# Kernel tuning notes

Hardware: AMD Instinct MI355X
Metric: run time of the kernel (lower is better)

## Reference

```python
import jax, jax.numpy as jnp
import numpy as np

NEG_INF = -1e30  # stand-in for float('-inf') masked_fill (safe for softmax)


def setup_inputs() -> dict:
    key = jax.random.key(0)
    ks = jax.random.split(key, 7)
    B, T, C, H, D = 4, 2048, 64, 6, 64
    s = 1.0 / np.sqrt(C)
    return {
        "x": jax.random.normal(ks[0], (B, T, C), dtype=jnp.float32),
        "y": jax.random.normal(ks[1], (B, T, C), dtype=jnp.float32),
        "Wq": jax.random.normal(ks[2], (H, C, D), dtype=jnp.float32) * s,
        "Wk": jax.random.normal(ks[3], (H, C, D), dtype=jnp.float32) * s,
        "Wv": jax.random.normal(ks[4], (H, C, D), dtype=jnp.float32) * s,
        "W_proj": jax.random.normal(ks[5], (H * D, C), dtype=jnp.float32) * (1.0 / np.sqrt(H * D)),
        "b_proj": jnp.zeros((C,), dtype=jnp.float32),
    }


def reference(x, y, Wq, Wk, Wv, W_proj, b_proj):
    # x, y: [B, T, C]; per-head projections stacked over H (heads vectorized).
    B, T, C = x.shape
    H, _, D = Wq.shape
    q = jnp.einsum("btc,hcd->bhtd", x, Wq)   # query from decoder input x
    k = jnp.einsum("btc,hcd->bhtd", y, Wk)   # key from encoder output y
    v = jnp.einsum("btc,hcd->bhtd", y, Wv)
    scale = D ** (-0.5)
    wei = jnp.einsum("bhtd,bhsd->bhts", q, k) * scale  # [B,H,T,T]
    # triu(ones(T,T), diagonal=1) future mask (causal)
    future = jnp.triu(jnp.ones((T, T), dtype=bool), k=1)
    wei = jnp.where(future, NEG_INF, wei)
    wei = jax.nn.softmax(wei, axis=-1)  # dropout = identity in eval
    out = jnp.einsum("bhts,bhsd->bhtd", wei, v)          # [B,H,T,D]
    out = out.transpose(0, 2, 1, 3).reshape(B, T, H * D)  # concat heads
    return out @ W_proj + b_proj                          # [B,T,C]
```

## Files before the change

### kernel.cpp

```cpp
#include <hip/hip_runtime.h>


typedef unsigned short u16t;
typedef __attribute__((ext_vector_type(8))) short short8;
typedef __attribute__((ext_vector_type(4))) float float4v;

#define MFMA16(a, b, c) __builtin_amdgcn_mfma_f32_16x16x32_bf16((a), (b), (c), 0, 0, 0)

union U8 { short8 s; unsigned u[4]; };

__device__ __forceinline__ float fexp2(float x) {
  return __builtin_amdgcn_exp2f(x);
}
__device__ __forceinline__ float bf2f(u16t u) {
  return __uint_as_float(((unsigned)u) << 16);
}
__device__ __forceinline__ u16t f2bf(float f) {
  unsigned u = __float_as_uint(f);
  u += 0x7fffu + ((u >> 16) & 1u);
  return (u16t)(u >> 16);
}
__device__ __forceinline__ unsigned bftr(float f) {
  return __float_as_uint(f) >> 16;
}
__device__ __forceinline__ short8 load8_f32_bf16(const float* p) {
  float4 f0 = *(const float4*)p;
  float4 f1 = *(const float4*)(p + 4);
  short8 r;
  r[0] = (short)f2bf(f0.x); r[1] = (short)f2bf(f0.y);
  r[2] = (short)f2bf(f0.z); r[3] = (short)f2bf(f0.w);
  r[4] = (short)f2bf(f1.x); r[5] = (short)f2bf(f1.y);
  r[6] = (short)f2bf(f1.z); r[7] = (short)f2bf(f1.w);
  return r;
}

constexpr int Bb = 4, Tt = 2048, Cc = 64, Hh = 6, Dd = 64;
constexpr int BH = Bb * Hh;
constexpr int NQT = Tt / 64;
constexpr int LDT = 72;
constexpr int LDV = 136;
constexpr int OST = 68;
#define QSCALE (0.125f * 1.44269504088896f)

__global__ __launch_bounds__(256) void qkv_kernel(
    const float* __restrict__ x, const float* __restrict__ y,
    const float* __restrict__ Wq, const float* __restrict__ Wk,
    const float* __restrict__ Wv,
    u16t* __restrict__ Q, u16t* __restrict__ K, u16t* __restrict__ Vt) {
  __shared__ __align__(16) u16t wtq[64 * LDT];
  __shared__ __align__(16) u16t wtk[64 * LDT];
  __shared__ __align__(16) u16t wtv[64 * LDT];

  int bid = blockIdx.x;
  int bh = bid >> 5, tt = bid & 31;
  int b = bh / Hh, h = bh - b * Hh;
  int tid = threadIdx.x;
  int w = tid >> 6, lane = tid & 63;
  int l15 = lane & 15, q4 = lane >> 4;

  {
    const float4* wq4 = (const float4*)(Wq + h * 4096);
    const float4* wk4 = (const float4*)(Wk + h * 4096);
    const float4* wv4 = (const float4*)(Wv + h * 4096);
#pragma unroll
    for (int i = 0; i < 4; ++i) {
      int fidx = tid + i * 256;
      float4 qv = wq4[fidx], kv = wk4[fidx], vv = wv4[fidx];
      int base = fidx * 4;
      int c = base >> 6, d0 = base & 63;
      wtq[(d0 + 0) * LDT + c] = f2bf(qv.x);
      wtq[(d0 + 1) * LDT + c] = f2bf(qv.y);
      wtq[(d0 + 2) * LDT + c] = f2bf(qv.z);
      wtq[(d0 + 3) * LDT + c] = f2bf(qv.w);
      wtk[(d0 + 0) * LDT + c] = f2bf(kv.x);
      wtk[(d0 + 1) * LDT + c] = f2bf(kv.y);
      wtk[(d0 + 2) * LDT + c] = f2bf(kv.z);
      wtk[(d0 + 3) * LDT + c] = f2bf(kv.w);
      wtv[(d0 + 0) * LDT + c] = f2bf(vv.x);
      wtv[(d0 + 1) * LDT + c] = f2bf(vv.y);
      wtv[(d0 + 2) * LDT + c] = f2bf(vv.z);
      wtv[(d0 + 3) * LDT + c] = f2bf(vv.w);
    }
  }

  int trow = tt * 64 + w * 16 + l15;
  const float* xrow = x + ((size_t)b * Tt + trow) * Cc;
  const float* yrow = y + ((size_t)b * Tt + trow) * Cc;
  short8 xa[2], ya[2];
#pragma unroll
  for (int kc = 0; kc < 2; ++kc) {
    xa[kc] = load8_f32_bf16(xrow + kc * 32 + q4 * 8);
    ya[kc] = load8_f32_bf16(yrow + kc * 32 + q4 * 8);
  }
  __syncthreads();

  float4v qa4[4], ka4[4], va4[4];
#pragma unroll
  for (int nc = 0; nc < 4; ++nc) {
    qa4[nc] = (float4v){0.f, 0.f, 0.f, 0.f};
    ka4[nc] = (float4v){0.f, 0.f, 0.f, 0.f};
    va4[nc] = (float4v){0.f, 0.f, 0.f, 0.f};
  }
#pragma unroll
  for (int nc = 0; nc < 4; ++nc) {
#pragma unroll
    for (int kc = 0; kc < 2; ++kc) {
      int off = (nc * 16 + l15) * LDT + kc * 32 + q4 * 8;
      short8 bq = *(const short8*)&wtq[off];
      short8 bk = *(const short8*)&wtk[off];
      short8 bv = *(const short8*)&wtv[off];
      qa4[nc] = MFMA16(xa[kc], bq, qa4[nc]);
      ka4[nc] = MFMA16(ya[kc], bk, ka4[nc]);
      va4[nc] = MFMA16(ya[kc], bv, va4[nc]);
    }
  }
  __syncthreads();

#pragma unroll
  for (int reg = 0; reg < 4; ++reg) {
    int rloc = w * 16 + q4 * 4 + reg;
#pragma unroll
    for (int nc = 0; nc < 4; ++nc) {
      wtq[rloc * LDT + nc * 16 + l15] = f2bf(qa4[nc][reg] * QSCALE);
      wtk[rloc * LDT + nc * 16 + l15] = f2bf(ka4[nc][reg]);
      wtv[(nc * 16 + l15) * LDT + rloc] = f2bf(va4[nc][reg]);
    }
  }
  __syncthreads();

  size_t tilebase = ((size_t)bh * Tt + tt * 64) * Dd;
#pragma unroll
  for (int i = 0; i < 2; ++i) {
    int id = tid * 2 + i;
    int row = id >> 3, c8 = id & 7;
    *(uint4*)&Q[tilebase + row * 64 + c8 * 8] = *(const uint4*)&wtq[row * LDT + c8 * 8];
    *(uint4*)&K[tilebase + row * 64 + c8 * 8] = *(const uint4*)&wtk[row * LDT + c8 * 8];
    *(uint4*)&Vt[((size_t)bh * 64 + row) * Tt + tt * 64 + c8 * 8] =
        *(const uint4*)&wtv[row * LDT + c8 * 8];
  }
}

__global__ __launch_bounds__(256) void attn_kernel(
    const u16t* __restrict__ Q, const u16t* __restrict__ K,
    const u16t* __restrict__ Vt, u16t* __restrict__ att) {
  __shared__ __align__(16) unsigned char smem[128 * LDT * 2 + 64 * LDV * 2];
  u16t* Kl = (u16t*)smem;
  u16t* Vl = (u16t*)(smem + 128 * LDT * 2);
  float* Ol = (float*)smem;
  float* Ll = (float*)(smem + 64 * OST * 4);

  int bid = blockIdx.x;
  int bh = bid % BH;
  int qt = (NQT - 1) - bid / BH;
  int b = bh / Hh, h = bh - (bh / Hh) * Hh;
  int tid = threadIdx.x;
  int w = tid >> 6;
  int lane = tid & 63;
  int l15 = lane & 15, q4 = lane >> 4;

  short8 qf[4][2];
#pragma unroll
  for (int it = 0; it < 4; ++it) {
    const u16t* qb = Q + ((size_t)bh * Tt + qt * 64 + it * 16 + l15) * Dd;
    qf[it][0] = *(const short8*)(qb + q4 * 8);
    qf[it][1] = *(const short8*)(qb + 32 + q4 * 8);
  }

  float4v O[4][4];
#pragma unroll
  for (int it = 0; it < 4; ++it)
#pragma unroll
    for (int nc = 0; nc < 4; ++nc) O[it][nc] = (float4v){0.f, 0.f, 0.f, 0.f};
  float l_[4] = {0.f, 0.f, 0.f, 0.f};

  const u16t* Kbh = K + (size_t)bh * Tt * Dd;
  const u16t* Vbh = Vt + (size_t)bh * Dd * Tt;
  const int bsmax = qt >> 1;

  for (int bs = 0; bs <= bsmax; ++bs) {
    __syncthreads();
    {
      const u16t* ks = Kbh + (size_t)bs * 128 * 64;
      const u16t* vs = Vbh + bs * 128;
#pragma unroll
      for (int i = 0; i < 4; ++i) {
        int id = tid + i * 256;
        *(uint4*)&Kl[(id >> 3) * LDT + (id & 7) * 8] =
            *(const uint4*)(ks + (size_t)(id >> 3) * 64 + (id & 7) * 8);
        *(uint4*)&Vl[(id >> 4) * LDV + (id & 15) * 8] =
            *(const uint4*)(vs + (size_t)(id >> 4) * Tt + (id & 15) * 8);
      }
    }
    __syncthreads();

    bool d0 = (2 * bs == qt);
    bool s1 = (2 * bs + 1 > qt);
    bool d1 = (2 * bs + 1 == qt);

    short8 kf00 = *(const short8*)&Kl[(w * 16 + l15) * LDT + q4 * 8];
    short8 kf01 = *(const short8*)&Kl[(w * 16 + l15) * LDT + 32 + q4 * 8];
    short8 kf10 = kf00, kf11 = kf01;
    if (!s1) {
      kf10 = *(const short8*)&Kl[(64 + w * 16 + l15) * LDT + q4 * 8];
      kf11 = *(const short8*)&Kl[(64 + w * 16 + l15) * LDT + 32 + q4 * 8];
    }
    short8 vf[4];
#pragma unroll
    for (int nc = 0; nc < 4; ++nc) {
      U8 t;
      *(uint2*)&t.u[0] = *(const uint2*)&Vl[(nc * 16 + l15) * LDV + w * 16 + q4 * 4];
      *(uint2*)&t.u[2] = *(const uint2*)&Vl[(nc * 16 + l15) * LDV + 64 + w * 16 + q4 * 4];
      vf[nc] = t.s;
    }

#pragma unroll
    for (int it = 0; it < 4; ++it) {
      if (d0 && w > it) continue;
      float4v S0 = (float4v){0.f, 0.f, 0.f, 0.f};
      S0 = MFMA16(kf00, qf[it][0], S0);
      S0 = MFMA16(kf01, qf[it][1], S0);
      bool m0 = d0 && (w == it);
      float p0[4], p1[4];
#pragma unroll
      for (int reg = 0; reg < 4; ++reg) {
        p0[reg] = (m0 && (q4 * 4 + reg) > l15) ? 0.f : fexp2(S0[reg]);
        l_[it] += p0[reg];
      }
      if (s1 || (d1 && w > it)) {
#pragma unroll
        for (int reg = 0; reg < 4; ++reg) p1[reg] = 0.f;
      } else {
        float4v S1 = (float4v){0.f, 0.f, 0.f, 0.f};
        S1 = MFMA16(kf10, qf[it][0], S1);
        S1 = MFMA16(kf11, qf[it][1], S1);
        bool m1 = d1 && (w == it);
#pragma unroll
        for (int reg = 0; reg < 4; ++reg) {
          p1[reg] = (m1 && (q4 * 4 + reg) > l15) ? 0.f : fexp2(S1[reg]);
          l_[it] += p1[reg];
        }
      }
      U8 pa;
      pa.u[0] = bftr(p0[0]) | (bftr(p0[1]) << 16);
      pa.u[1] = bftr(p0[2]) | (bftr(p0[3]) << 16);
      pa.u[2] = bftr(p1[0]) | (bftr(p1[1]) << 16);
      pa.u[3] = bftr(p1[2]) | (bftr(p1[3]) << 16);
#pragma unroll
      for (int nc = 0; nc < 4; ++nc)
        O[it][nc] = MFMA16(pa.s, vf[nc], O[it][nc]);
    }
  }

#pragma unroll
  for (int it = 0; it < 4; ++it) {
    l_[it] += __shfl_xor(l_[it], 16);
    l_[it] += __shfl_xor(l_[it], 32);
  }

  __syncthreads();
#pragma unroll
  for (int rr = 0; rr < 4; ++rr) {
#pragma unroll
    for (int itc = 0; itc < 4; ++itc) {
      if (((itc - w) & 3) == rr) {
#pragma unroll
        for (int nc = 0; nc < 4; ++nc)
#pragma unroll
          for (int reg = 0; reg < 4; ++reg) {
            int addr = (itc * 16 + q4 * 4 + reg) * OST + nc * 16 + l15;
            if (rr == 0) Ol[addr] = O[itc][nc][reg];
            else         Ol[addr] += O[itc][nc][reg];
          }
        if (q4 == 0) {
          if (rr == 0) Ll[itc * 16 + l15] = l_[itc];
          else         Ll[itc * 16 + l15] += l_[itc];
        }
      }
    }
    __syncthreads();
  }

#pragma unroll
  for (int i = 0; i < 2; ++i) {
    int id = tid * 2 + i;
    int row = id >> 3, c8 = id & 7;
    float inv = 1.0f / Ll[row];
    const float* orow = &Ol[row * OST + c8 * 8];
    U8 o;
#pragma unroll
    for (int k = 0; k < 4; ++k)
      o.u[k] = f2bf(orow[2 * k] * inv) | ((unsigned)f2bf(orow[2 * k + 1] * inv) << 16);
    int t = qt * 64 + row;
    *(uint4*)&att[((size_t)b * Tt + t) * (Hh * Dd) + h * Dd + c8 * 8] = *(const uint4*)&o;
  }
}

constexpr int LDP = 392;

__global__ __launch_bounds__(256) void proj_kernel(
    const u16t* __restrict__ att, const float* __restrict__ Wp,
    const float* __restrict__ bp, float* __restrict__ out) {
  __shared__ __align__(16) u16t wpt[64 * LDP];

  int bid = blockIdx.x;
  int tid = threadIdx.x;
  int w = tid >> 6, lane = tid & 63;
  int l15 = lane & 15, q4 = lane >> 4;

  const float4* wp4 = (const float4*)Wp;
#pragma unroll
  for (int i = 0; i < 24; ++i) {
    int fidx = tid + i * 256;
    float4 v = wp4[fidx];
    int base = fidx * 4;
    int r = base >> 6, c0 = base & 63;
    wpt[(c0 + 0) * LDP + r] = f2bf(v.x);
    wpt[(c0 + 1) * LDP + r] = f2bf(v.y);
    wpt[(c0 + 2) * LDP + r] = f2bf(v.z);
    wpt[(c0 + 3) * LDP + r] = f2bf(v.w);
  }
  __syncthreads();

  int row0 = bid * 64 + w * 16;
  const u16t* arow = att + (size_t)(row0 + l15) * 384;

  float4v acc[4];
#pragma unroll
  for (int nc = 0; nc < 4; ++nc) acc[nc] = (float4v){0.f, 0.f, 0.f, 0.f};

#pragma unroll
  for (int kc = 0; kc < 12; ++kc) {
    short8 a = *(const short8*)(arow + kc * 32 + q4 * 8);
#pragma unroll
    for (int nc = 0; nc < 4; ++nc) {
      short8 bfr = *(const short8*)&wpt[(nc * 16 + l15) * LDP + kc * 32 + q4 * 8];
      acc[nc] = MFMA16(a, bfr, acc[nc]);
    }
  }

  float bv[4];
#pragma unroll
  for (int nc = 0; nc < 4; ++nc) bv[nc] = bp[nc * 16 + l15];
#pragma unroll
  for (int reg = 0; reg < 4; ++reg) {
    int t = row0 + q4 * 4 + reg;
    size_t obase = (size_t)t * 64;
#pragma unroll
    for (int nc = 0; nc < 4; ++nc)
      out[obase + nc * 16 + l15] = acc[nc][reg] + bv[nc];
  }
}

extern "C" void kernel_launch(void* const* d_in, const int* in_sizes, int n_in,
                              void* d_out, int out_size, void* d_ws, size_t ws_size,
                              hipStream_t stream) {
  const float* x  = (const float*)d_in[0];
  const float* y  = (const float*)d_in[1];
  const float* Wq = (const float*)d_in[2];
  const float* Wk = (const float*)d_in[3];
  const float* Wv = (const float*)d_in[4];
  const float* Wp = (const float*)d_in[5];
  const float* bp = (const float*)d_in[6];
  float* out = (float*)d_out;

  const size_t NBH = (size_t)BH * Tt * Dd;
  u16t* Qs   = (u16t*)d_ws;
  u16t* Ks   = Qs + NBH;
  u16t* Vts  = Ks + NBH;
  u16t* attb = Vts + NBH;

  qkv_kernel<<<BH * NQT, 256, 0, stream>>>(x, y, Wq, Wk, Wv, Qs, Ks, Vts);
  attn_kernel<<<BH * NQT, 256, 0, stream>>>(Qs, Ks, Vts, attb);
  proj_kernel<<<(Bb * Tt) / 64, 256, 0, stream>>>(attb, Wp, bp, out);
}
```

Measured before the change: 121.4 us.

## Load K/V tiles directly into LDS with XOR-swizzled layout

Replaces the register-staged global-to-LDS copy of K and V tiles with global_load_lds direct transfers. Since these loads cannot pad rows, the producer kernel now writes K and Vt with an XOR swizzle on 16-byte chunks, and the attention kernel reads fragments with matching swizzled indices to avoid LDS bank conflicts. This removes VGPR round-trips and the padded-stride layout, but couples the two kernels' layouts and relies on the swizzle arithmetic being correct for the V fragment reads.

New measurement: 121.7 us. Within noise of the previous version (+0.3%).

```diff
diff --git a/kernel.cpp b/kernel.cpp
--- a/kernel.cpp
+++ b/kernel.cpp
@@ -33,12 +33,16 @@
   r[6] = (short)f2bf(f1.z); r[7] = (short)f2bf(f1.w);
   return r;
 }
+__device__ __forceinline__ void gload16(const u16t* g, u16t* l) {
+  __builtin_amdgcn_global_load_lds(
+      (const __attribute__((address_space(1))) unsigned int*)g,
+      (__attribute__((address_space(3))) unsigned int*)l, 16, 0, 0);
+}
 
 constexpr int Bb = 4, Tt = 2048, Cc = 64, Hh = 6, Dd = 64;
 constexpr int BH = Bb * Hh;
 constexpr int NQT = Tt / 64;
 constexpr int LDT = 72;
-constexpr int LDV = 136;
 constexpr int OST = 68;
 #define QSCALE (0.125f * 1.44269504088896f)
 
@@ -134,8 +138,9 @@
     int id = tid * 2 + i;
     int row = id >> 3, c8 = id & 7;
     *(uint4*)&Q[tilebase + row * 64 + c8 * 8] = *(const uint4*)&wtq[row * LDT + c8 * 8];
-    *(uint4*)&K[tilebase + row * 64 + c8 * 8] = *(const uint4*)&wtk[row * LDT + c8 * 8];
-    *(uint4*)&Vt[((size_t)bh * 64 + row) * Tt + tt * 64 + c8 * 8] =
+    *(uint4*)&K[tilebase + row * 64 + ((c8 ^ (row & 7)) * 8)] =
+        *(const uint4*)&wtk[row * LDT + c8 * 8];
+    *(uint4*)&Vt[((size_t)bh * 64 + row) * Tt + tt * 64 + ((c8 ^ (row & 7)) * 8)] =
         *(const uint4*)&wtv[row * LDT + c8 * 8];
   }
 }
@@ -143,9 +148,9 @@
 __global__ __launch_bounds__(256) void attn_kernel(
     const u16t* __restrict__ Q, const u16t* __restrict__ K,
     const u16t* __restrict__ Vt, u16t* __restrict__ att) {
-  __shared__ __align__(16) unsigned char smem[128 * LDT * 2 + 64 * LDV * 2];
+  __shared__ __align__(16) unsigned char smem[128 * 64 * 2 + 64 * 128 * 2 + 512];
   u16t* Kl = (u16t*)smem;
-  u16t* Vl = (u16t*)(smem + 128 * LDT * 2);
+  u16t* Vl = (u16t*)(smem + 128 * 64 * 2);
   float* Ol = (float*)smem;
   float* Ll = (float*)(smem + 64 * OST * 4);
 
@@ -157,6 +162,7 @@
   int w = tid >> 6;
   int lane = tid & 63;
   int l15 = lane & 15, q4 = lane >> 4;
+  int e7 = l15 & 7;
 
   short8 qf[4][2];
 #pragma unroll
@@ -180,15 +186,14 @@
   for (int bs = 0; bs <= bsmax; ++bs) {
     __syncthreads();
     {
-      const u16t* ks = Kbh + (size_t)bs * 128 * 64;
+      const u16t* ks = Kbh + (size_t)bs * 8192;
       const u16t* vs = Vbh + bs * 128;
 #pragma unroll
       for (int i = 0; i < 4; ++i) {
-        int id = tid + i * 256;
-        *(uint4*)&Kl[(id >> 3) * LDT + (id & 7) * 8] =
-            *(const uint4*)(ks + (size_t)(id >> 3) * 64 + (id & 7) * 8);
-        *(uint4*)&Vl[(id >> 4) * LDV + (id & 15) * 8] =
-            *(const uint4*)(vs + (size_t)(id >> 4) * Tt + (id & 15) * 8);
+        int cid = (w * 4 + i) * 64 + lane;
+        gload16(ks + cid * 8, &Kl[(w * 4 + i) * 512]);
+        gload16(vs + (size_t)(cid >> 4) * Tt + (cid & 15) * 8,
+                &Vl[(w * 4 + i) * 512]);
       }
     }
     __syncthreads();
@@ -197,19 +202,20 @@
     bool s1 = (2 * bs + 1 > qt);
     bool d1 = (2 * bs + 1 == qt);
 
-    short8 kf00 = *(const short8*)&Kl[(w * 16 + l15) * LDT + q4 * 8];
-    short8 kf01 = *(const short8*)&Kl[(w * 16 + l15) * LDT + 32 + q4 * 8];
+    short8 kf00 = *(const short8*)&Kl[(w * 16 + l15) * 64 + ((q4 ^ e7) * 8)];
+    short8 kf01 = *(const short8*)&Kl[(w * 16 + l15) * 64 + (((4 + q4) ^ e7) * 8)];
     short8 kf10 = kf00, kf11 = kf01;
     if (!s1) {
-      kf10 = *(const short8*)&Kl[(64 + w * 16 + l15) * LDT + q4 * 8];
-      kf11 = *(const short8*)&Kl[(64 + w * 16 + l15) * LDT + 32 + q4 * 8];
+      kf10 = *(const short8*)&Kl[(64 + w * 16 + l15) * 64 + ((q4 ^ e7) * 8)];
+      kf11 = *(const short8*)&Kl[(64 + w * 16 + l15) * 64 + (((4 + q4) ^ e7) * 8)];
     }
     short8 vf[4];
+    int st = (((w * 4 + q4) >> 1) ^ e7) * 8 + (q4 & 1) * 4;
 #pragma unroll
     for (int nc = 0; nc < 4; ++nc) {
       U8 t;
-      *(uint2*)&t.u[0] = *(const uint2*)&Vl[(nc * 16 + l15) * LDV + w * 16 + q4 * 4];
-      *(uint2*)&t.u[2] = *(const uint2*)&Vl[(nc * 16 + l15) * LDV + 64 + w * 16 + q4 * 4];
+      *(uint2*)&t.u[0] = *(const uint2*)&Vl[(nc * 16 + l15) * 128 + st];
+      *(uint2*)&t.u[2] = *(const uint2*)&Vl[(nc * 16 + l15) * 128 + 64 + st];
       vf[nc] = t.s;
     }
 
```

## Process two query tiles per attention block to share K/V tile loads

Applied to the files above, without the earlier changes.

Each attention block now covers two adjacent 64-row query tiles. The four warps are split into two query tiles times two halves of each 128-key block, so every K/V tile staged in shared memory serves 128 query rows instead of 64. This is meant to halve the redundant global-to-LDS K/V traffic and barrier overhead per query row. In exchange the grid shrinks to half as many larger blocks, which can hurt load balance across CUs under the causal triangle. The cross-warp reduction of partial outputs and row sums is reworked for the new warp split.

Result: slower. 154.6 us (+27.4%).

```diff
diff --git a/kernel.cpp b/kernel.cpp
--- a/kernel.cpp
+++ b/kernel.cpp
@@ -147,21 +147,24 @@
   u16t* Kl = (u16t*)smem;
   u16t* Vl = (u16t*)(smem + 128 * LDT * 2);
   float* Ol = (float*)smem;
-  float* Ll = (float*)(smem + 64 * OST * 4);
+  float* Ll = (float*)(smem + 2 * 64 * OST * 4);
 
   int bid = blockIdx.x;
   int bh = bid % BH;
-  int qt = (NQT - 1) - bid / BH;
+  int p = 15 - bid / BH;
   int b = bh / Hh, h = bh - (bh / Hh) * Hh;
   int tid = threadIdx.x;
   int w = tid >> 6;
   int lane = tid & 63;
   int l15 = lane & 15, q4 = lane >> 4;
+  int wt = w >> 1;
+  int wp = w & 1;
+  int qtile = 2 * p + wt;
 
   short8 qf[4][2];
 #pragma unroll
   for (int it = 0; it < 4; ++it) {
-    const u16t* qb = Q + ((size_t)bh * Tt + qt * 64 + it * 16 + l15) * Dd;
+    const u16t* qb = Q + ((size_t)bh * Tt + qtile * 64 + it * 16 + l15) * Dd;
     qf[it][0] = *(const short8*)(qb + q4 * 8);
     qf[it][1] = *(const short8*)(qb + 32 + q4 * 8);
   }
@@ -175,12 +178,11 @@
 
   const u16t* Kbh = K + (size_t)bh * Tt * Dd;
   const u16t* Vbh = Vt + (size_t)bh * Dd * Tt;
-  const int bsmax = qt >> 1;
-
-  for (int bs = 0; bs <= bsmax; ++bs) {
+
+  for (int bs = 0; bs <= p; ++bs) {
     __syncthreads();
     {
-      const u16t* ks = Kbh + (size_t)bs * 128 * 64;
+      const u16t* ks = Kbh + (size_t)bs * 8192;
       const u16t* vs = Vbh + bs * 128;
 #pragma unroll
       for (int i = 0; i < 4; ++i) {
@@ -193,61 +195,65 @@
     }
     __syncthreads();
 
-    bool d0 = (2 * bs == qt);
-    bool s1 = (2 * bs + 1 > qt);
-    bool d1 = (2 * bs + 1 == qt);
-
-    short8 kf00 = *(const short8*)&Kl[(w * 16 + l15) * LDT + q4 * 8];
-    short8 kf01 = *(const short8*)&Kl[(w * 16 + l15) * LDT + 32 + q4 * 8];
-    short8 kf10 = kf00, kf11 = kf01;
-    if (!s1) {
-      kf10 = *(const short8*)&Kl[(64 + w * 16 + l15) * LDT + q4 * 8];
-      kf11 = *(const short8*)&Kl[(64 + w * 16 + l15) * LDT + 32 + q4 * 8];
-    }
-    short8 vf[4];
-#pragma unroll
-    for (int nc = 0; nc < 4; ++nc) {
-      U8 t;
-      *(uint2*)&t.u[0] = *(const uint2*)&Vl[(nc * 16 + l15) * LDV + w * 16 + q4 * 4];
-      *(uint2*)&t.u[2] = *(const uint2*)&Vl[(nc * 16 + l15) * LDV + 64 + w * 16 + q4 * 4];
-      vf[nc] = t.s;
-    }
-
-#pragma unroll
-    for (int it = 0; it < 4; ++it) {
-      if (d0 && w > it) continue;
-      float4v S0 = (float4v){0.f, 0.f, 0.f, 0.f};
-      S0 = MFMA16(kf00, qf[it][0], S0);
-      S0 = MFMA16(kf01, qf[it][1], S0);
-      bool m0 = d0 && (w == it);
-      float p0[4], p1[4];
-#pragma unroll
-      for (int reg = 0; reg < 4; ++reg) {
-        p0[reg] = (m0 && (q4 * 4 + reg) > l15) ? 0.f : fexp2(S0[reg]);
-        l_[it] += p0[reg];
+    int gb = bs * 8 + wp * 4;
+    int tb = qtile * 4;
+
+#pragma unroll
+    for (int m = 0; m < 2; ++m) {
+      int s0 = wp * 4 + 2 * m;
+      int gs0 = gb + 2 * m, gs1 = gs0 + 1;
+      if (gs0 > tb + 3) continue;
+
+      short8 k0a = *(const short8*)&Kl[(s0 * 16 + l15) * LDT + q4 * 8];
+      short8 k0b = *(const short8*)&Kl[(s0 * 16 + l15) * LDT + 32 + q4 * 8];
+      short8 k1a = *(const short8*)&Kl[((s0 + 1) * 16 + l15) * LDT + q4 * 8];
+      short8 k1b = *(const short8*)&Kl[((s0 + 1) * 16 + l15) * LDT + 32 + q4 * 8];
+      short8 vf[4];
+#pragma unroll
+      for (int nc = 0; nc < 4; ++nc) {
+        U8 t;
+        *(uint2*)&t.u[0] = *(const uint2*)&Vl[(nc * 16 + l15) * LDV + s0 * 16 + q4 * 4];
+        *(uint2*)&t.u[2] = *(const uint2*)&Vl[(nc * 16 + l15) * LDV + (s0 + 1) * 16 + q4 * 4];
+        vf[nc] = t.s;
       }
-      if (s1 || (d1 && w > it)) {
-#pragma unroll
-        for (int reg = 0; reg < 4; ++reg) p1[reg] = 0.f;
-      } else {
-        float4v S1 = (float4v){0.f, 0.f, 0.f, 0.f};
-        S1 = MFMA16(kf10, qf[it][0], S1);
-        S1 = MFMA16(kf11, qf[it][1], S1);
-        bool m1 = d1 && (w == it);
+
+#pragma unroll
+      for (int it = 0; it < 4; ++it) {
+        int git = tb + it;
+        if (gs0 > git) continue;
+        float4v S0 = (float4v){0.f, 0.f, 0.f, 0.f};
+        S0 = MFMA16(k0a, qf[it][0], S0);
+        S0 = MFMA16(k0b, qf[it][1], S0);
+        bool m0 = (gs0 == git);
+        float p0[4], p1[4];
 #pragma unroll
         for (int reg = 0; reg < 4; ++reg) {
-          p1[reg] = (m1 && (q4 * 4 + reg) > l15) ? 0.f : fexp2(S1[reg]);
-          l_[it] += p1[reg];
+          p0[reg] = (m0 && (q4 * 4 + reg) > l15) ? 0.f : fexp2(S0[reg]);
+          l_[it] += p0[reg];
         }
+        if (gs1 > git) {
+#pragma unroll
+          for (int reg = 0; reg < 4; ++reg) p1[reg] = 0.f;
+        } else {
+          float4v S1 = (float4v){0.f, 0.f, 0.f, 0.f};
+          S1 = MFMA16(k1a, qf[it][0], S1);
+          S1 = MFMA16(k1b, qf[it][1], S1);
+          bool m1 = (gs1 == git);
+#pragma unroll
+          for (int reg = 0; reg < 4; ++reg) {
+            p1[reg] = (m1 && (q4 * 4 + reg) > l15) ? 0.f : fexp2(S1[reg]);
+            l_[it] += p1[reg];
+          }
+        }
+        U8 pa;
+        pa.u[0] = bftr(p0[0]) | (bftr(p0[1]) << 16);
+        pa.u[1] = bftr(p0[2]) | (bftr(p0[3]) << 16);
+        pa.u[2] = bftr(p1[0]) | (bftr(p1[1]) << 16);
+        pa.u[3] = bftr(p1[2]) | (bftr(p1[3]) << 16);
+#pragma unroll
+        for (int nc = 0; nc < 4; ++nc)
+          O[it][nc] = MFMA16(pa.s, vf[nc], O[it][nc]);
       }
-      U8 pa;
-      pa.u[0] = bftr(p0[0]) | (bftr(p0[1]) << 16);
-      pa.u[1] = bftr(p0[2]) | (bftr(p0[3]) << 16);
-      pa.u[2] = bftr(p1[0]) | (bftr(p1[1]) << 16);
-      pa.u[3] = bftr(p1[2]) | (bftr(p1[3]) << 16);
-#pragma unroll
-      for (int nc = 0; nc < 4; ++nc)
-        O[it][nc] = MFMA16(pa.s, vf[nc], O[it][nc]);
     }
   }
 
@@ -259,21 +265,22 @@
 
   __syncthreads();
 #pragma unroll
-  for (int rr = 0; rr < 4; ++rr) {
+  for (int rr = 0; rr < 2; ++rr) {
 #pragma unroll
     for (int itc = 0; itc < 4; ++itc) {
-      if (((itc - w) & 3) == rr) {
+      if ((((itc >> 1) ^ wp) & 1) == rr) {
 #pragma unroll
         for (int nc = 0; nc < 4; ++nc)
 #pragma unroll
           for (int reg = 0; reg < 4; ++reg) {
-            int addr = (itc * 16 + q4 * 4 + reg) * OST + nc * 16 + l15;
+            int addr = (wt * 64 + itc * 16 + q4 * 4 + reg) * OST + nc * 16 + l15;
             if (rr == 0) Ol[addr] = O[itc][nc][reg];
             else         Ol[addr] += O[itc][nc][reg];
           }
         if (q4 == 0) {
-          if (rr == 0) Ll[itc * 16 + l15] = l_[itc];
-          else         Ll[itc * 16 + l15] += l_[itc];
+          int la = wt * 64 + itc * 16 + l15;
+          if (rr == 0) Ll[la] = l_[itc];
+          else         Ll[la] += l_[itc];
         }
       }
     }
@@ -281,16 +288,16 @@
   }
 
 #pragma unroll
-  for (int i = 0; i < 2; ++i) {
-    int id = tid * 2 + i;
-    int row = id >> 3, c8 = id & 7;
-    float inv = 1.0f / Ll[row];
-    const float* orow = &Ol[row * OST + c8 * 8];
+  for (int i = 0; i < 4; ++i) {
+    int id = tid + i * 256;
+    int tile = id >> 9, row = (id >> 3) & 63, c8 = id & 7;
+    float inv = 1.0f / Ll[tile * 64 + row];
+    const float* orow = &Ol[(tile * 64 + row) * OST + c8 * 8];
     U8 o;
 #pragma unroll
     for (int k = 0; k < 4; ++k)
       o.u[k] = f2bf(orow[2 * k] * inv) | ((unsigned)f2bf(orow[2 * k + 1] * inv) << 16);
-    int t = qt * 64 + row;
+    int t = (2 * p + tile) * 64 + row;
     *(uint4*)&att[((size_t)b * Tt + t) * (Hh * Dd) + h * Dd + c8 * 8] = *(const uint4*)&o;
   }
 }
@@ -370,6 +377,6 @@
   u16t* attb = Vts + NBH;
 
   qkv_kernel<<<BH * NQT, 256, 0, stream>>>(x, y, Wq, Wk, Wv, Qs, Ks, Vts);
-  attn_kernel<<<BH * NQT, 256, 0, stream>>>(Qs, Ks, Vts, attb);
+  attn_kernel<<<BH * 16, 256, 0, stream>>>(Qs, Ks, Vts, attb);
   proj_kernel<<<(Bb * Tt) / 64, 256, 0, stream>>>(attb, Wp, bp, out);
 }
```
